# Kernel optimization log

Measured on AMD Instinct MI355X. Metric: run time of the kernel, lower is better.

Reference implementation:

```python
import jax, jax.numpy as jnp
import numpy as np

N, E, F_IN, D_HID, H, N_CLS = 50000, 800000, 128, 96, 8, 40
DH = D_HID // H  # 12
NEG_SLOPE = 0.2


def setup_inputs() -> dict:
    key = jax.random.key(0)
    ks = jax.random.split(key, 14)
    x = jax.random.normal(ks[0], (N, F_IN), dtype=jnp.float32)
    edge_src = jax.random.randint(ks[1], (E,), 0, N, dtype=jnp.int32)
    edge_dst = jax.random.randint(ks[2], (E,), 0, N, dtype=jnp.int32)
    s = 0.1  # keep attention logits in a stable range
    W0 = jax.random.normal(ks[3], (F_IN, D_HID), dtype=jnp.float32) * s
    as0 = jax.random.normal(ks[4], (H, DH), dtype=jnp.float32) * s
    ad0 = jax.random.normal(ks[5], (H, DH), dtype=jnp.float32) * s
    b0 = jnp.zeros((D_HID,), dtype=jnp.float32)
    W1 = jax.random.normal(ks[6], (D_HID, D_HID), dtype=jnp.float32) * s
    as1 = jax.random.normal(ks[7], (H, DH), dtype=jnp.float32) * s
    ad1 = jax.random.normal(ks[8], (H, DH), dtype=jnp.float32) * s
    b1 = jnp.zeros((D_HID,), dtype=jnp.float32)
    Wout = jax.random.normal(ks[9], (D_HID, N_CLS), dtype=jnp.float32) * s
    bout = jnp.zeros((N_CLS,), dtype=jnp.float32)
    return dict(x=x, edge_src=edge_src, edge_dst=edge_dst, W0=W0, as0=as0,
                ad0=ad0, b0=b0, W1=W1, as1=as1, ad1=ad1, b1=b1,
                Wout=Wout, bout=bout)


def _gat_conv(x, src, dst, W, a_src, a_dst, b):
    """PyG-style GATConv: per-head linear, edge attention, segment softmax, scatter-sum."""
    n = x.shape[0]
    h = (x @ W).reshape(n, H, DH)                       # [N, H, Dh]
    alpha_s = jnp.einsum('nhd,hd->nh', h, a_src)        # [N, H]
    alpha_d = jnp.einsum('nhd,hd->nh', h, a_dst)        # [N, H]
    e = alpha_s[src] + alpha_d[dst]                     # [E, H]
    e = jnp.where(e > 0, e, NEG_SLOPE * e)              # LeakyReLU(0.2)
    # numerically-stable segment softmax over edges grouped by destination
    m = jax.ops.segment_max(e, dst, num_segments=n)     # [N, H]
    m = jnp.where(jnp.isfinite(m), m, 0.0)
    p = jnp.exp(e - m[dst])                             # [E, H]
    z = jax.ops.segment_sum(p, dst, num_segments=n)     # [N, H]
    alpha = p / (z[dst] + 1e-16)                        # [E, H]
    msg = h[src] * alpha[:, :, None]                    # [E, H, Dh]
    out = jax.ops.segment_sum(msg, dst, num_segments=n) # [N, H, Dh]
    return out.reshape(n, H * DH) + b


def reference(x, edge_src, edge_dst, W0, as0, ad0, b0, W1, as1, ad1, b1, Wout, bout):
    src = edge_src.astype(jnp.int32)
    dst = edge_dst.astype(jnp.int32)
    h = _gat_conv(x, src, dst, W0, as0, ad0, b0)                 # input_fc (no activation)
    h = jax.nn.relu(_gat_conv(h, src, dst, W1, as1, ad1, b1))    # conv layer + ReLU (eval: no dropout)
    out = h @ Wout + bout
    return jax.nn.log_softmax(out, axis=1)
```

## Files before the change

### kernel.cpp

```cpp
#include <hip/hip_runtime.h>
#include <hip/hip_fp16.h>
#include <math.h>

#define N_NODES 50000
#define N_EDGES 800000
#define F_IN    128
#define D_HID   96
#define NHEAD   8
#define DH      12
#define N_CLS   40
#define NEG_SLOPE 0.2f

#define NPART   (N_NODES / 8)
#define CKS     64
#define CHK     (N_EDGES / CKS)
#define NHB     (8 * CKS)

#define GBM 64
#define NGB ((N_NODES + GBM - 1) / GBM)
#define WPAD 136

#define HALFN   (N_NODES / 2)
#define AGG_NPB 32
#define NAGGB   ((HALFN + AGG_NPB - 1) / AGG_NPB)

typedef _Float16 f16x8 __attribute__((ext_vector_type(8)));
typedef float    f32x4 __attribute__((ext_vector_type(4)));

template<bool A16>
__device__ __forceinline__ void gemm_alpha_mfma_body(
    const void* __restrict__ Av, const float* __restrict__ W,
    const float* __restrict__ asrc, const float* __restrict__ adst,
    uint4* __restrict__ Hrec,
    int M, int K, int bid,
    _Float16 (*Wt)[WPAD], _Float16 (*Hl)[104], float* avl, float* adl)
{
    int tid  = threadIdx.x;
    int lane = tid & 63;
    int w    = tid >> 6;
    int n0   = bid * GBM;

    for (int idx = tid; idx < K * 96; idx += 256) {
        int k = idx / 96, n = idx - k * 96;
        Wt[n][k] = (_Float16)W[idx];
    }
    if (tid < 96) { avl[tid] = asrc[tid]; adl[tid] = adst[tid]; }
    __syncthreads();

    int c  = lane & 15;
    int kg = lane >> 4;
    int arow = n0 + (w << 4) + c;
    int ar = arow < M ? arow : M - 1;

    f32x4 acc[6];
#pragma unroll
    for (int t = 0; t < 6; t++) acc[t] = (f32x4){0.f, 0.f, 0.f, 0.f};

    for (int k0 = 0; k0 < K; k0 += 32) {
        f16x8 av;
        if constexpr (A16) {
            const _Float16* ap = (const _Float16*)Av + (size_t)ar * K + (kg << 3);
            av = *(const f16x8*)(ap + k0);
        } else {
            const float* ap = (const float*)Av + (size_t)ar * K + (kg << 3);
            float4 a0 = *(const float4*)(ap + k0);
            float4 a1 = *(const float4*)(ap + k0 + 4);
            av[0] = (_Float16)a0.x; av[1] = (_Float16)a0.y;
            av[2] = (_Float16)a0.z; av[3] = (_Float16)a0.w;
            av[4] = (_Float16)a1.x; av[5] = (_Float16)a1.y;
            av[6] = (_Float16)a1.z; av[7] = (_Float16)a1.w;
        }
#pragma unroll
        for (int t = 0; t < 6; t++) {
            f16x8 bv = *(const f16x8*)&Wt[t * 16 + c][k0 + (kg << 3)];
            acc[t] = __builtin_amdgcn_mfma_f32_16x16x32_f16(av, bv, acc[t], 0, 0, 0);
        }
    }

    int rbase = (w << 4) + (kg << 2);
#pragma unroll
    for (int t = 0; t < 6; t++)
#pragma unroll
        for (int r = 0; r < 4; r++)
            Hl[rbase + r][t * 16 + c] = (_Float16)acc[t][r];
    __syncthreads();

    int row = tid >> 2, q = tid & 3;
    int gr = n0 + row;
    if (gr < M) {
        float s0 = 0.f, s1 = 0.f, d0 = 0.f, d1 = 0.f;
#pragma unroll
        for (int j = 0; j < 12; j++) {
            float f = (float)Hl[row][q * 24 + j];
            s0 += f * avl[q * 24 + j];
            d0 += f * adl[q * 24 + j];
        }
#pragma unroll
        for (int j = 12; j < 24; j++) {
            float f = (float)Hl[row][q * 24 + j];
            s1 += f * avl[q * 24 + j];
            d1 += f * adl[q * 24 + j];
        }
        const uint* hp = (const uint*)&Hl[row][q * 24];
        uint4* rec = Hrec + ((size_t)q * N_NODES + gr) * 4;
        rec[0] = make_uint4(__float_as_uint(s0), hp[0], hp[1], hp[2]);
        rec[1] = make_uint4(hp[3], hp[4], hp[5], __float_as_uint(d0));
        rec[2] = make_uint4(__float_as_uint(s1), hp[6], hp[7], hp[8]);
        rec[3] = make_uint4(hp[9], hp[10], hp[11], __float_as_uint(d1));
    }
}

__global__ __launch_bounds__(256) void hist_gemm_kernel(
    const int* __restrict__ edst, unsigned short* __restrict__ Hmat,
    const float* __restrict__ A, const float* __restrict__ W0,
    const float* __restrict__ asrc, const float* __restrict__ adst,
    uint4* __restrict__ Hrec)
{
    __shared__ __align__(16) char smem[40448];
    if (blockIdx.x < NHB) {
        int* lh = (int*)smem;
        int g = blockIdx.x & 7, c = blockIdx.x >> 3;
        int lo = g * NPART;
        for (int i = threadIdx.x; i < NPART; i += 256) lh[i] = 0;
        __syncthreads();
        const int4* d4 = (const int4*)(edst + c * CHK);
        for (int i = threadIdx.x; i < CHK / 4; i += 256) {
            int4 dv = d4[i];
            int a = dv.x - lo, b = dv.y - lo, cc = dv.z - lo, dd = dv.w - lo;
            if ((unsigned)a  < (unsigned)NPART) atomicAdd(&lh[a], 1);
            if ((unsigned)b  < (unsigned)NPART) atomicAdd(&lh[b], 1);
            if ((unsigned)cc < (unsigned)NPART) atomicAdd(&lh[cc], 1);
            if ((unsigned)dd < (unsigned)NPART) atomicAdd(&lh[dd], 1);
        }
        __syncthreads();
        unsigned int* hrow = (unsigned int*)(Hmat + (size_t)c * N_NODES + lo);
        for (int i = threadIdx.x; i < NPART / 2; i += 256)
            hrow[i] = (unsigned)lh[2 * i] | ((unsigned)lh[2 * i + 1] << 16);
    } else {
        _Float16 (*Wt)[WPAD] = (_Float16(*)[WPAD])smem;
        _Float16 (*Hl)[104]  = (_Float16(*)[104])(smem + 26112);
        float* avl = (float*)(smem + 26112 + 13312);
        float* adl = avl + 96;
        gemm_alpha_mfma_body<false>(A, W0, asrc, adst, Hrec, N_NODES, F_IN,
                                    blockIdx.x - NHB, Wt, Hl, avl, adl);
    }
}

__global__ __launch_bounds__(256) void gemm_alpha_kernel(
    const _Float16* __restrict__ A, const float* __restrict__ W1,
    const float* __restrict__ asrc, const float* __restrict__ adst,
    uint4* __restrict__ Hrec, int M, int K)
{
    __shared__ __align__(16) char smem[40448];
    _Float16 (*Wt)[WPAD] = (_Float16(*)[WPAD])smem;
    _Float16 (*Hl)[104]  = (_Float16(*)[104])(smem + 26112);
    float* avl = (float*)(smem + 26112 + 13312);
    float* adl = avl + 96;
    gemm_alpha_mfma_body<true>(A, W1, asrc, adst, Hrec, M, K, blockIdx.x,
                               Wt, Hl, avl, adl);
}

__global__ void scan1_kernel(const unsigned short* __restrict__ Hmat,
                             int* __restrict__ incl,
                             int* __restrict__ partials, int n) {
    __shared__ int sdata[256];
    int t = threadIdx.x;
    int base = blockIdx.x * 1024 + t * 4;
    int v[4] = {0, 0, 0, 0};
    if (base + 4 <= n) {
        for (int c = 0; c < CKS; c++) {
            ushort4 h = *(const ushort4*)&Hmat[(size_t)c * N_NODES + base];
            v[0] += h.x; v[1] += h.y; v[2] += h.z; v[3] += h.w;
        }
    } else if (base < n) {
        for (int c = 0; c < CKS; c++)
#pragma unroll
            for (int j = 0; j < 4; j++)
                if (base + j < n) v[j] += Hmat[(size_t)c * N_NODES + base + j];
    }
    v[1] += v[0]; v[2] += v[1]; v[3] += v[2];
    sdata[t] = v[3];
    __syncthreads();
    for (int off = 1; off < 256; off <<= 1) {
        int x = (t >= off) ? sdata[t - off] : 0;
        __syncthreads();
        sdata[t] += x;
        __syncthreads();
    }
    int excl = sdata[t] - v[3];
#pragma unroll
    for (int j = 0; j < 4; j++) { int i = base + j; if (i < n) incl[i] = v[j] + excl; }
    if (t == 255) partials[blockIdx.x] = sdata[255];
}

__global__ void scan3_kernel(const int* __restrict__ incl,
                             const int* __restrict__ partials,
                             const unsigned short* __restrict__ Hmat,
                             unsigned short* __restrict__ Bmat16,
                             int* __restrict__ rowptr,
                             int n, int nb) {
    int i = blockIdx.x * blockDim.x + threadIdx.x;
    if (i >= n) return;
    int myb = i >> 10;
    int psum = 0;
    for (int b = 0; b < nb; b++) psum += (b < myb) ? partials[b] : 0;
    int v = incl[i] + psum;
    rowptr[i + 1] = v;
    if (i == 0) rowptr[0] = 0;
    int running = 0;
    for (int c = 0; c < CKS; c++) {
        Bmat16[(size_t)c * N_NODES + i] = (unsigned short)running;
        running += Hmat[(size_t)c * N_NODES + i];
    }
}

__global__ __launch_bounds__(256) void fill_kernel(
    const int* __restrict__ esrc, const int* __restrict__ edst,
    const int* __restrict__ rowptr, const unsigned short* __restrict__ Bmat16,
    unsigned short* __restrict__ srclist)
{
    __shared__ int cur[NPART];
    int g = blockIdx.x & 7, c = blockIdx.x >> 3;
    int lo = g * NPART;
    const unsigned short* rrow = Bmat16 + (size_t)c * N_NODES + lo;
    const int* rp = rowptr + lo;
    for (int i = threadIdx.x; i < NPART; i += 256) cur[i] = rp[i] + rrow[i];
    __syncthreads();
    int base = c * CHK;
    const int4* d4 = (const int4*)(edst + base);
    const int4* s4 = (const int4*)(esrc + base);
    for (int i = threadIdx.x; i < CHK / 4; i += 256) {
        int4 dv = d4[i], sv = s4[i];
        int a = dv.x - lo, b = dv.y - lo, cc = dv.z - lo, dd = dv.w - lo;
        if ((unsigned)a < (unsigned)NPART) {
            int p = atomicAdd(&cur[a], 1); srclist[p] = (unsigned short)sv.x;
        }
        if ((unsigned)b < (unsigned)NPART) {
            int p = atomicAdd(&cur[b], 1); srclist[p] = (unsigned short)sv.y;
        }
        if ((unsigned)cc < (unsigned)NPART) {
            int p = atomicAdd(&cur[cc], 1); srclist[p] = (unsigned short)sv.z;
        }
        if ((unsigned)dd < (unsigned)NPART) {
            int p = atomicAdd(&cur[dd], 1); srclist[p] = (unsigned short)sv.w;
        }
    }
}

__device__ __forceinline__ void agg_rec(const uint4* __restrict__ rp, float ad,
                                        float& z, float* acc) {
    uint4 u0 = rp[0], u1 = rp[1];
    float e = __uint_as_float(u0.x) + ad;
    e = (e > 0.f) ? e : NEG_SLOPE * e;
    float p = __expf(e);
    z += p;
    float2 f0 = __half22float2(*(const __half2*)&u0.y);
    float2 f1 = __half22float2(*(const __half2*)&u0.z);
    float2 f2 = __half22float2(*(const __half2*)&u0.w);
    float2 f3 = __half22float2(*(const __half2*)&u1.x);
    float2 f4 = __half22float2(*(const __half2*)&u1.y);
    float2 f5 = __half22float2(*(const __half2*)&u1.z);
    acc[0] += p * f0.x; acc[1]  += p * f0.y;
    acc[2] += p * f1.x; acc[3]  += p * f1.y;
    acc[4] += p * f2.x; acc[5]  += p * f2.y;
    acc[6] += p * f3.x; acc[7]  += p * f3.y;
    acc[8] += p * f4.x; acc[9]  += p * f4.y;
    acc[10] += p * f5.x; acc[11] += p * f5.y;
}

__global__ __launch_bounds__(256) void gat_aggregate_kernel(
    const uint4* __restrict__ Hrec,
    const int* __restrict__ rowptr, const unsigned short* __restrict__ srclist,
    const float* __restrict__ bias,
    _Float16* __restrict__ outYh, float* __restrict__ outY, int mode)
{
    int s    = blockIdx.x & 7;
    int g    = s >> 1;
    int half = s & 1;
    int local = (blockIdx.x >> 3) * AGG_NPB + (threadIdx.x >> 3);
    if (local >= HALFN) return;
    int n   = half * HALFN + local;
    int l   = threadIdx.x & 7;
    int hh2 = l & 1;
    int j   = l >> 1;

    const uint4* gtab = Hrec + (size_t)g * N_NODES * 4;
    float ad = __uint_as_float(gtab[(size_t)n * 4 + hh2 * 2 + 1].w);

    int s0 = rowptr[n], s1 = rowptr[n + 1];
    float z = 0.f;
    float acc[12];
#pragma unroll
    for (int t = 0; t < 12; t++) acc[t] = 0.f;

    int i = s0 + j;
    for (; i + 12 < s1; i += 16) {
        int sa = srclist[i];
        int sb = srclist[i + 4];
        int sc = srclist[i + 8];
        int sd = srclist[i + 12];
        agg_rec(gtab + (size_t)sa * 4 + hh2 * 2, ad, z, acc);
        agg_rec(gtab + (size_t)sb * 4 + hh2 * 2, ad, z, acc);
        agg_rec(gtab + (size_t)sc * 4 + hh2 * 2, ad, z, acc);
        agg_rec(gtab + (size_t)sd * 4 + hh2 * 2, ad, z, acc);
    }
    for (; i < s1; i += 4) {
        int sa = srclist[i];
        agg_rec(gtab + (size_t)sa * 4 + hh2 * 2, ad, z, acc);
    }

#pragma unroll
    for (int m = 2; m <= 4; m <<= 1) {
        z += __shfl_xor(z, m, 64);
#pragma unroll
        for (int t = 0; t < 12; t++) acc[t] += __shfl_xor(acc[t], m, 64);
    }

    if (j == 0) {
        float inv = 1.f / (z + 1e-16f);
        const float* bp = bias + g * 24 + hh2 * 12;
        float o[12];
#pragma unroll
        for (int t = 0; t < 12; t++) o[t] = acc[t] * inv + bp[t];
        if (mode == 0) {
            uint ww[6];
#pragma unroll
            for (int t = 0; t < 6; t++) {
                __half2 hv = __floats2half2_rn(o[2 * t], o[2 * t + 1]);
                ww[t] = *(const uint*)&hv;
            }
            uint2* yp = (uint2*)(outYh + (size_t)n * D_HID + g * 24 + hh2 * 12);
            yp[0] = make_uint2(ww[0], ww[1]);
            yp[1] = make_uint2(ww[2], ww[3]);
            yp[2] = make_uint2(ww[4], ww[5]);
        } else {
#pragma unroll
            for (int t = 0; t < 12; t++) o[t] = fmaxf(o[t], 0.f);
            float4* op = (float4*)(outY + (size_t)n * D_HID + g * 24 + hh2 * 12);
            op[0] = make_float4(o[0], o[1], o[2], o[3]);
            op[1] = make_float4(o[4], o[5], o[6], o[7]);
            op[2] = make_float4(o[8], o[9], o[10], o[11]);
        }
    }
}

__global__ __launch_bounds__(256) void out_lsm_kernel(
    const float* __restrict__ X, const float* __restrict__ Wout,
    const float* __restrict__ bout, float* __restrict__ out)
{
    __shared__ float Ws[D_HID * N_CLS];
    __shared__ float bs[N_CLS];
    for (int i = threadIdx.x; i < D_HID * N_CLS; i += 256) Ws[i] = Wout[i];
    for (int i = threadIdx.x; i < N_CLS; i += 256) bs[i] = bout[i];
    __syncthreads();

    int n = blockIdx.x * blockDim.x + threadIdx.x;
    if (n >= N_NODES) return;

    float acc[N_CLS];
#pragma unroll
    for (int c = 0; c < N_CLS; c++) acc[c] = bs[c];

    const float4* xp = (const float4*)(X + (size_t)n * D_HID);
    for (int k4 = 0; k4 < D_HID / 4; k4++) {
        float4 xv = xp[k4];
        const float* wrow = &Ws[(k4 * 4) * N_CLS];
#pragma unroll
        for (int c4 = 0; c4 < N_CLS / 4; c4++) {
            float4 wa = *(const float4*)(wrow + c4 * 4);
            float4 wb = *(const float4*)(wrow + N_CLS + c4 * 4);
            float4 wc = *(const float4*)(wrow + 2 * N_CLS + c4 * 4);
            float4 wd = *(const float4*)(wrow + 3 * N_CLS + c4 * 4);
            acc[c4 * 4 + 0] += xv.x * wa.x + xv.y * wb.x + xv.z * wc.x + xv.w * wd.x;
            acc[c4 * 4 + 1] += xv.x * wa.y + xv.y * wb.y + xv.z * wc.y + xv.w * wd.y;
            acc[c4 * 4 + 2] += xv.x * wa.z + xv.y * wb.z + xv.z * wc.z + xv.w * wd.z;
            acc[c4 * 4 + 3] += xv.x * wa.w + xv.y * wb.w + xv.z * wc.w + xv.w * wd.w;
        }
    }

    float m = acc[0];
#pragma unroll
    for (int c = 1; c < N_CLS; c++) m = fmaxf(m, acc[c]);
    float s = 0.f;
#pragma unroll
    for (int c = 0; c < N_CLS; c++) s += __expf(acc[c] - m);
    float lg = __logf(s);

    float4* op = (float4*)(out + (size_t)n * N_CLS);
#pragma unroll
    for (int c4 = 0; c4 < N_CLS / 4; c4++) {
        op[c4] = make_float4(acc[c4 * 4 + 0] - m - lg, acc[c4 * 4 + 1] - m - lg,
                             acc[c4 * 4 + 2] - m - lg, acc[c4 * 4 + 3] - m - lg);
    }
}

extern "C" void kernel_launch(void* const* d_in, const int* in_sizes, int n_in,
                              void* d_out, int out_size, void* d_ws, size_t ws_size,
                              hipStream_t stream)
{
    const float* x    = (const float*)d_in[0];
    const int*   esrc = (const int*)d_in[1];
    const int*   edst = (const int*)d_in[2];
    const float* W0   = (const float*)d_in[3];
    const float* as0  = (const float*)d_in[4];
    const float* ad0  = (const float*)d_in[5];
    const float* b0   = (const float*)d_in[6];
    const float* W1   = (const float*)d_in[7];
    const float* as1  = (const float*)d_in[8];
    const float* ad1  = (const float*)d_in[9];
    const float* b1   = (const float*)d_in[10];
    const float* Wout = (const float*)d_in[11];
    const float* bout = (const float*)d_in[12];
    float* out = (float*)d_out;

    char* p = (char*)d_ws;
    float*    bufY  = (float*)p;    p += (size_t)N_NODES * D_HID * sizeof(float);
    _Float16* bufYh = (_Float16*)p; p += (size_t)N_NODES * D_HID * sizeof(_Float16);
    uint4*    Hrec  = (uint4*)p;    p += (size_t)4 * N_NODES * 64;
    int*   rowptr = (int*)p;   p += ((size_t)N_NODES + 16) * sizeof(int);
    int*   incl   = (int*)p;   p += ((size_t)N_NODES + 16) * sizeof(int);
    unsigned short* srclist = (unsigned short*)p; p += (size_t)N_EDGES * sizeof(unsigned short);
    int*   partials = (int*)p; p += 256;

    unsigned short* Hmat   = (unsigned short*)bufYh;
    unsigned short* Bmat16 = (unsigned short*)bufY;

    int nscan = (N_NODES + 1023) / 1024;

    hist_gemm_kernel<<<NHB + NGB, 256, 0, stream>>>(
        edst, Hmat, x, W0, as0, ad0, Hrec);
    scan1_kernel<<<nscan, 256, 0, stream>>>(Hmat, incl, partials, N_NODES);
    scan3_kernel<<<(N_NODES + 255) / 256, 256, 0, stream>>>(
        incl, partials, Hmat, Bmat16, rowptr, N_NODES, nscan);
    fill_kernel<<<NHB, 256, 0, stream>>>(esrc, edst, rowptr, Bmat16, srclist);
    gat_aggregate_kernel<<<8 * NAGGB, 256, 0, stream>>>(
        Hrec, rowptr, srclist, b0, bufYh, bufY, 0);
    gemm_alpha_kernel<<<NGB, 256, 0, stream>>>(
        bufYh, W1, as1, ad1, Hrec, N_NODES, D_HID);
    gat_aggregate_kernel<<<8 * NAGGB, 256, 0, stream>>>(
        Hrec, rowptr, srclist, b1, bufYh, bufY, 1);
    out_lsm_kernel<<<(N_NODES + 255) / 256, 256, 0, stream>>>(bufY, Wout, bout, out);
}
```

Measured before the change: 161.2 us.

## Sort nodes by in-degree to balance per-wave work in GAT aggregation

A per-chunk in-degree histogram is built in scan1, and a new single-block kernel turns it into bucket offsets. scan3 then writes a permutation of node ids grouped by capped degree. Both aggregation kernels take nodes in this permuted order, so neighbouring thread groups in a wave handle nodes of similar degree, which is meant to cut idle lanes from uneven edge loops. The cost is an extra launch, extra atomics and scan work, and less regular memory access for the per-node reads and output writes.

```diff
diff --git a/kernel.cpp b/kernel.cpp
--- a/kernel.cpp
+++ b/kernel.cpp
@@ -23,6 +23,8 @@
 #define HALFN   (N_NODES / 2)
 #define AGG_NPB 32
 #define NAGGB   ((HALFN + AGG_NPB - 1) / AGG_NPB)
+
+#define NCH     196
 
 typedef _Float16 f16x8 __attribute__((ext_vector_type(8)));
 typedef float    f32x4 __attribute__((ext_vector_type(4)));
@@ -162,9 +164,13 @@
 
 __global__ void scan1_kernel(const unsigned short* __restrict__ Hmat,
                              int* __restrict__ incl,
-                             int* __restrict__ partials, int n) {
+                             int* __restrict__ partials,
+                             int* __restrict__ Dhist, int n) {
     __shared__ int sdata[256];
+    __shared__ int dh[4 * 256];
     int t = threadIdx.x;
+    for (int k = t; k < 1024; k += 256) dh[k] = 0;
+    __syncthreads();
     int base = blockIdx.x * 1024 + t * 4;
     int v[4] = {0, 0, 0, 0};
     if (base + 4 <= n) {
@@ -178,6 +184,10 @@
             for (int j = 0; j < 4; j++)
                 if (base + j < n) v[j] += Hmat[(size_t)c * N_NODES + base + j];
     }
+    int sc = t >> 6;
+#pragma unroll
+    for (int j = 0; j < 4; j++)
+        if (base + j < n) atomicAdd(&dh[sc * 256 + (v[j] > 255 ? 255 : v[j])], 1);
     v[1] += v[0]; v[2] += v[1]; v[3] += v[2];
     sdata[t] = v[3];
     __syncthreads();
@@ -191,27 +201,59 @@
 #pragma unroll
     for (int j = 0; j < 4; j++) { int i = base + j; if (i < n) incl[i] = v[j] + excl; }
     if (t == 255) partials[blockIdx.x] = sdata[255];
+    for (int k = t; k < 1024; k += 256)
+        Dhist[blockIdx.x * 1024 + k] = dh[k];
+}
+
+__global__ void dbase_kernel(const int* __restrict__ Dhist, int* __restrict__ dbase) {
+    __shared__ int sdata[256];
+    int b = threadIdx.x;
+    int tot = 0;
+    for (int c = 0; c < NCH; c++) tot += Dhist[c * 256 + b];
+    sdata[b] = tot;
+    __syncthreads();
+    for (int off = 1; off < 256; off <<= 1) {
+        int x = (b >= off) ? sdata[b - off] : 0;
+        __syncthreads();
+        sdata[b] += x;
+        __syncthreads();
+    }
+    int run = sdata[b] - tot;
+    for (int c = 0; c < NCH; c++) {
+        dbase[c * 256 + b] = run;
+        run += Dhist[c * 256 + b];
+    }
 }
 
 __global__ void scan3_kernel(const int* __restrict__ incl,
                              const int* __restrict__ partials,
                              const unsigned short* __restrict__ Hmat,
+                             const int* __restrict__ dbase,
                              unsigned short* __restrict__ Bmat16,
                              int* __restrict__ rowptr,
+                             unsigned short* __restrict__ perm,
                              int n, int nb) {
-    int i = blockIdx.x * blockDim.x + threadIdx.x;
+    __shared__ int cur[256];
+    int t = threadIdx.x;
+    cur[t] = dbase[blockIdx.x * 256 + t];
+    __syncthreads();
+    int i = blockIdx.x * blockDim.x + t;
     if (i >= n) return;
     int myb = i >> 10;
     int psum = 0;
     for (int b = 0; b < nb; b++) psum += (b < myb) ? partials[b] : 0;
-    int v = incl[i] + psum;
+    int iv = incl[i];
+    int v = iv + psum;
     rowptr[i + 1] = v;
     if (i == 0) rowptr[0] = 0;
+    int deg = ((i & 1023) == 0) ? iv : iv - incl[i - 1];
     int running = 0;
     for (int c = 0; c < CKS; c++) {
         Bmat16[(size_t)c * N_NODES + i] = (unsigned short)running;
         running += Hmat[(size_t)c * N_NODES + i];
     }
+    int pos = atomicAdd(&cur[deg > 255 ? 255 : deg], 1);
+    perm[pos] = (unsigned short)i;
 }
 
 __global__ __launch_bounds__(256) void fill_kernel(
@@ -271,15 +313,16 @@
 __global__ __launch_bounds__(256) void gat_aggregate_kernel(
     const uint4* __restrict__ Hrec,
     const int* __restrict__ rowptr, const unsigned short* __restrict__ srclist,
+    const unsigned short* __restrict__ perm,
     const float* __restrict__ bias,
     _Float16* __restrict__ outYh, float* __restrict__ outY, int mode)
 {
     int s    = blockIdx.x & 7;
     int g    = s >> 1;
     int half = s & 1;
-    int local = (blockIdx.x >> 3) * AGG_NPB + (threadIdx.x >> 3);
-    if (local >= HALFN) return;
-    int n   = half * HALFN + local;
+    int p_s  = (blockIdx.x >> 3) * AGG_NPB + (threadIdx.x >> 3);
+    if (p_s >= HALFN) return;
+    int n   = perm[p_s * 2 + half];
     int l   = threadIdx.x & 7;
     int hh2 = l & 1;
     int j   = l >> 1;
@@ -421,6 +464,9 @@
     int*   incl   = (int*)p;   p += ((size_t)N_NODES + 16) * sizeof(int);
     unsigned short* srclist = (unsigned short*)p; p += (size_t)N_EDGES * sizeof(unsigned short);
     int*   partials = (int*)p; p += 256;
+    int*   Dhist  = (int*)p;   p += (size_t)NCH * 256 * sizeof(int);
+    int*   dbase  = (int*)p;   p += (size_t)NCH * 256 * sizeof(int);
+    unsigned short* perm = (unsigned short*)p; p += (size_t)N_NODES * sizeof(unsigned short);
 
     unsigned short* Hmat   = (unsigned short*)bufYh;
     unsigned short* Bmat16 = (unsigned short*)bufY;
@@ -429,15 +475,16 @@
 
     hist_gemm_kernel<<<NHB + NGB, 256, 0, stream>>>(
         edst, Hmat, x, W0, as0, ad0, Hrec);
-    scan1_kernel<<<nscan, 256, 0, stream>>>(Hmat, incl, partials, N_NODES);
+    scan1_kernel<<<nscan, 256, 0, stream>>>(Hmat, incl, partials, Dhist, N_NODES);
+    dbase_kernel<<<1, 256, 0, stream>>>(Dhist, dbase);
     scan3_kernel<<<(N_NODES + 255) / 256, 256, 0, stream>>>(
-        incl, partials, Hmat, Bmat16, rowptr, N_NODES, nscan);
+        incl, partials, Hmat, dbase, Bmat16, rowptr, perm, N_NODES, nscan);
     fill_kernel<<<NHB, 256, 0, stream>>>(esrc, edst, rowptr, Bmat16, srclist);
     gat_aggregate_kernel<<<8 * NAGGB, 256, 0, stream>>>(
-        Hrec, rowptr, srclist, b0, bufYh, bufY, 0);
+        Hrec, rowptr, srclist, perm, b0, bufYh, bufY, 0);
     gemm_alpha_kernel<<<NGB, 256, 0, stream>>>(
         bufYh, W1, as1, ad1, Hrec, N_NODES, D_HID);
     gat_aggregate_kernel<<<8 * NAGGB, 256, 0, stream>>>(
-        Hrec, rowptr, srclist, b1, bufYh, bufY, 1);
+        Hrec, rowptr, srclist, perm, b1, bufYh, bufY, 1);
     out_lsm_kernel<<<(N_NODES + 255) / 256, 256, 0, stream>>>(bufY, Wout, bout, out);
 }
```

Result: slower. 181.1 us (+12.3%).
